# Performance work log

Hardware: AMD Instinct MI355X
Metric: run time of the kernel (lower is better)

The kernel has to match this reference:

```python
import jax, jax.numpy as jnp
import numpy as np

N_NODES = 100000
N_EDGES = 1600000
IN_CH = 16
HID = 128
N_LAYERS = 4
OUT_CH = 3


def setup_inputs() -> dict:
    key = jax.random.key(0)
    ks = jax.random.split(key, 8)
    x = jax.random.normal(ks[0], (N_NODES, IN_CH), dtype=jnp.float32)
    edge_index = jax.random.randint(ks[1], (2, N_EDGES), 0, N_NODES, dtype=jnp.int64)
    # glorot-ish scaled params
    enc_W = jax.random.normal(ks[2], (IN_CH, HID), dtype=jnp.float32) * (1.0 / np.sqrt(IN_CH))
    enc_b = jnp.zeros((HID,), dtype=jnp.float32)
    conv_W = jax.random.normal(ks[3], (N_LAYERS, HID, HID), dtype=jnp.float32) * (1.0 / np.sqrt(HID))
    conv_b = jnp.zeros((N_LAYERS, HID), dtype=jnp.float32)
    dec_W = jax.random.normal(ks[4], (HID, OUT_CH), dtype=jnp.float32) * (1.0 / np.sqrt(HID))
    dec_b = jnp.zeros((OUT_CH,), dtype=jnp.float32)
    return {"x": x, "edge_index": edge_index, "enc_W": enc_W, "enc_b": enc_b,
            "conv_W": conv_W, "conv_b": conv_b, "dec_W": dec_W, "dec_b": dec_b}


def _gcn_forward(x, edge_index, enc_W, enc_b, conv_W, conv_b, dec_W, dec_b):
    n = x.shape[0]
    # PyG GCNConv: add self-loops, symmetric deg^-1/2 normalization
    loops = jnp.arange(n, dtype=edge_index.dtype)
    src = jnp.concatenate([edge_index[0], loops])  # [E+N]
    dst = jnp.concatenate([edge_index[1], loops])  # [E+N]
    deg = jax.ops.segment_sum(jnp.ones_like(dst, dtype=x.dtype), dst, num_segments=n)
    dinv = jnp.where(deg > 0, jax.lax.rsqrt(deg), 0.0)
    norm = (dinv[src] * dinv[dst])[:, None]  # [E+N, 1]

    h = jax.nn.relu(x @ enc_W + enc_b)  # encoder + ReLU
    for l in range(conv_W.shape[0]):
        hw = h @ conv_W[l]                      # [N, H] transform
        msg = hw[src] * norm                    # gather + normalize
        h = jax.ops.segment_sum(msg, dst, num_segments=n) + conv_b[l]
        h = jax.nn.relu(h)
    return h @ dec_W + dec_b  # decoder [N, 3]


def reference(x, edge_index, enc_W, enc_b, conv_W, conv_b, dec_W, dec_b):
    return _gcn_forward(x, edge_index, enc_W, enc_b, conv_W, conv_b, dec_W, dec_b)
```

## Files before the change

kernel.cpp:

```cpp
#include <hip/hip_runtime.h>


typedef float f32x4 __attribute__((ext_vector_type(4)));
typedef _Float16 h8 __attribute__((ext_vector_type(8)));

#define BKT_CAP 6144


__global__ __launch_bounds__(256) void k_bin(const int* __restrict__ src, const int* __restrict__ dst,
                                             int* __restrict__ bcnt, unsigned* __restrict__ ebuf, int E, int NB) {
  __shared__ int hist[512];
  __shared__ int lofs[512];
  int tid = threadIdx.x;
  int base = blockIdx.x * 4096;
  for (int i = tid; i < NB; i += 256) hist[i] = 0;
  __syncthreads();
  unsigned rec[16];
  int bk[16];
#pragma unroll
  for (int j = 0; j < 16; j++) {
    int e = base + j * 256 + tid;
    bk[j] = -1;
    if (e < E) {
      int d = dst[e];
      rec[j] = ((unsigned)(d & 255) << 24) | (unsigned)src[e];
      bk[j] = d >> 8;
      atomicAdd(&hist[bk[j]], 1);
    }
  }
  __syncthreads();
  for (int i = tid; i < NB; i += 256) {
    int c = hist[i];
    lofs[i] = c ? atomicAdd(&bcnt[i], c) : 0;
    hist[i] = 0;
  }
  __syncthreads();
#pragma unroll
  for (int j = 0; j < 16; j++) {
    if (bk[j] >= 0) {
      int p = lofs[bk[j]] + atomicAdd(&hist[bk[j]], 1);
      if (p < BKT_CAP) ebuf[(size_t)bk[j] * BKT_CAP + p] = rec[j];
    }
  }
}

__global__ __launch_bounds__(512) void k_bscan(const int* __restrict__ bcnt, int* __restrict__ bbase,
                                               int* __restrict__ rp, int NB, int N, int E) {
  __shared__ int wsum[8];
  int tid = threadIdx.x;
  int v = (tid < NB) ? bcnt[tid] : 0;
  int l = tid & 63, w = tid >> 6;
  int s = v;
#pragma unroll
  for (int off = 1; off < 64; off <<= 1) { int t = __shfl_up(s, off); if (l >= off) s += t; }
  if (l == 63) wsum[w] = s;
  __syncthreads();
  int woff = 0;
  for (int i = 0; i < w; i++) woff += wsum[i];
  if (tid < NB) bbase[tid] = woff + s - v;
  if (tid == 0) rp[N] = E;
}

__global__ __launch_bounds__(256) void k_bfill(const unsigned* __restrict__ ebuf, const int* __restrict__ bcnt,
                                               const int* __restrict__ bbase, int* __restrict__ rp,
                                               float* __restrict__ dinv, int* __restrict__ col, int N) {
  __shared__ int h[256];
  __shared__ int wsum[4];
  int b = blockIdx.x, tid = threadIdx.x;
  h[tid] = 0;
  __syncthreads();
  int n = min(bcnt[b], BKT_CAP);
  int bb = bbase[b];
  const unsigned* eb = ebuf + (size_t)b * BKT_CAP;
  for (int i = tid; i < n; i += 256) atomicAdd(&h[eb[i] >> 24], 1);
  __syncthreads();
  int cntv = h[tid];
  int l = tid & 63, wv = tid >> 6;
  int s = cntv;
#pragma unroll
  for (int off = 1; off < 64; off <<= 1) { int t = __shfl_up(s, off); if (l >= off) s += t; }
  if (l == 63) wsum[wv] = s;
  __syncthreads();
  int woff = 0;
  for (int i = 0; i < wv; i++) woff += wsum[i];
  int lpre = woff + s - cntv;
  int d = (b << 8) + tid;
  if (d < N) {
    rp[d] = bb + lpre;
    dinv[d] = 1.0f / sqrtf((float)(cntv + 1));
  }
  __syncthreads();
  h[tid] = lpre;
  __syncthreads();
  for (int i = tid; i < n; i += 256) {
    unsigned r = eb[i];
    int dlow = r >> 24;
    int pos = bb + atomicAdd(&h[dlow], 1);
    col[pos] = (int)(r & 0xFFFFFFu);
  }
}

__global__ __launch_bounds__(128) void k_prep_w(const float* __restrict__ convW, _Float16* __restrict__ Whi,
                                                _Float16* __restrict__ Wlo) {
  int lk = blockIdx.x;
  int l = lk >> 7, k = lk & 127, c = threadIdx.x;
  float x = convW[((size_t)l * 128 + k) * 128 + c];
  _Float16 hi = (_Float16)x;
  _Float16 lo = (_Float16)((x - (float)hi) * 2048.0f);
  size_t o = ((size_t)l * 128 + c) * 128 + k;
  Whi[o] = hi;
  Wlo[o] = lo;
}


__global__ __launch_bounds__(256) void k_encoder(const float* __restrict__ x, const float* __restrict__ W,
                                                 const float* __restrict__ b, _Float16* __restrict__ H, int N) {
  int node = blockIdx.x * 2 + (threadIdx.x >> 7);
  int c = threadIdx.x & 127;
  if (node >= N) return;
  const float* xr = x + (size_t)node * 16;
  float acc = b[c];
#pragma unroll
  for (int k = 0; k < 16; k++) acc = fmaf(xr[k], W[k * 128 + c], acc);
  H[(size_t)node * 128 + c] = (_Float16)fmaxf(acc, 0.0f);
}

__global__ __launch_bounds__(512) void k_gemm_mfma(const _Float16* __restrict__ A, const _Float16* __restrict__ Whi,
                                                   const _Float16* __restrict__ Wlo, const float* __restrict__ dinv,
                                                   _Float16* __restrict__ B, int N) {
  __shared__ __align__(16) ushort lds[3 * 128 * 64];
  const int tid = threadIdx.x;
  const int row0 = blockIdx.x * 128;
  const int w = tid >> 6, l = tid & 63;
  const int wm = w >> 1, wn = w & 1;
  const int lr = l & 15, lg = l >> 4;

  f32x4 zero4 = {0.0f, 0.0f, 0.0f, 0.0f};
  f32x4 acc[2][4], acc2[2][4];
#pragma unroll
  for (int m = 0; m < 2; m++)
#pragma unroll
    for (int n = 0; n < 4; n++) { acc[m][n] = zero4; acc2[m][n] = zero4; }

  for (int half = 0; half < 2; half++) {
    uint4 v[6];
#pragma unroll
    for (int i = 0; i < 6; i++) {
      int g = tid + i * 512;
      int region = g >> 10;
      int idx = g & 1023;
      int row = idx >> 3;
      int c16 = idx & 7;
      const _Float16* srcb;
      int grow = row;
      bool valid = true;
      if (region == 0) { srcb = A; grow = row0 + row; valid = grow < N; }
      else if (region == 1) { srcb = Whi; }
      else { srcb = Wlo; }
      v[i] = valid ? *reinterpret_cast<const uint4*>(srcb + (size_t)grow * 128 + half * 64 + c16 * 8)
                   : uint4{0u, 0u, 0u, 0u};
    }
    if (half) __syncthreads();
#pragma unroll
    for (int i = 0; i < 6; i++) {
      int g = tid + i * 512;
      int region = g >> 10;
      int idx = g & 1023;
      int row = idx >> 3;
      int c16 = idx & 7;
      int byte_off = region * 16384 + ((row * 128 + c16 * 16) ^ ((row & 7) << 4));
      *reinterpret_cast<uint4*>(reinterpret_cast<char*>(lds) + byte_off) = v[i];
    }
    __syncthreads();

#pragma unroll
    for (int ksl = 0; ksl < 2; ksl++) {
      int kb = (ksl * 32 + lg * 8) * 2;
      h8 ah[2];
#pragma unroll
      for (int m = 0; m < 2; m++) {
        int row = wm * 32 + m * 16 + lr;
        int off = (row * 128 + kb) ^ ((row & 7) << 4);
        ah[m] = *reinterpret_cast<const h8*>(reinterpret_cast<char*>(lds) + off);
      }
      h8 wh[4], wl[4];
#pragma unroll
      for (int n = 0; n < 4; n++) {
        int colr = wn * 64 + n * 16 + lr;
        int off = (colr * 128 + kb) ^ ((colr & 7) << 4);
        wh[n] = *reinterpret_cast<const h8*>(reinterpret_cast<char*>(lds) + 16384 + off);
        wl[n] = *reinterpret_cast<const h8*>(reinterpret_cast<char*>(lds) + 32768 + off);
      }
#pragma unroll
      for (int m = 0; m < 2; m++)
#pragma unroll
        for (int n = 0; n < 4; n++) {
          acc2[m][n] = __builtin_amdgcn_mfma_f32_16x16x32_f16(ah[m], wl[n], acc2[m][n], 0, 0, 0);
          acc[m][n]  = __builtin_amdgcn_mfma_f32_16x16x32_f16(ah[m], wh[n], acc[m][n], 0, 0, 0);
        }
    }
  }

#pragma unroll
  for (int m = 0; m < 2; m++) {
    int rbase = row0 + wm * 32 + m * 16 + lg * 4;
#pragma unroll
    for (int r = 0; r < 4; r++) {
      int grow = rbase + r;
      if (grow < N) {
        float s = dinv[grow];
#pragma unroll
        for (int n = 0; n < 4; n++) {
          int colc = wn * 64 + n * 16 + lr;
          float val = acc[m][n][r] + 4.8828125e-4f * acc2[m][n][r];
          B[(size_t)grow * 128 + colc] = (_Float16)(val * s);
        }
      }
    }
  }
}

__global__ __launch_bounds__(256) void k_aggregate(const _Float16* __restrict__ B, const int* __restrict__ rp,
                                                   const int* __restrict__ col, const float* __restrict__ dinv,
                                                   const float* __restrict__ bias, _Float16* __restrict__ H,
                                                   const float* __restrict__ decW, const float* __restrict__ decb,
                                                   float* __restrict__ out, int last, int N) {
  int w = threadIdx.x >> 6, l = threadIdx.x & 63;
  int d = blockIdx.x * 4 + w;
  if (d >= N) return;
  int g = l >> 4, c16 = l & 15;
  int choff = c16 * 8;

  h8 z = {(_Float16)0, (_Float16)0, (_Float16)0, (_Float16)0,
          (_Float16)0, (_Float16)0, (_Float16)0, (_Float16)0};
  h8 a0 = z, a1 = z, a2 = z, a3 = z;

  if (g == 0)
    a1 += *reinterpret_cast<const h8*>(B + (size_t)d * 128 + choff);

  int e0 = rp[d], e1 = rp[d + 1];
  int len = e1 - e0;
  int q = (len + 3) >> 2;
  int a = e0 + g * q;
  int b = a + q; b = b < e1 ? b : e1;
  int i = a;
  for (; i + 3 < b; i += 4) {
    int s0 = col[i], s1 = col[i + 1], s2 = col[i + 2], s3 = col[i + 3];
    a0 += *reinterpret_cast<const h8*>(B + (size_t)s0 * 128 + choff);
    a1 += *reinterpret_cast<const h8*>(B + (size_t)s1 * 128 + choff);
    a2 += *reinterpret_cast<const h8*>(B + (size_t)s2 * 128 + choff);
    a3 += *reinterpret_cast<const h8*>(B + (size_t)s3 * 128 + choff);
  }
  if (i < b)     a0 += *reinterpret_cast<const h8*>(B + (size_t)col[i] * 128 + choff);
  if (i + 1 < b) a1 += *reinterpret_cast<const h8*>(B + (size_t)col[i + 1] * 128 + choff);
  if (i + 2 < b) a2 += *reinterpret_cast<const h8*>(B + (size_t)col[i + 2] * 128 + choff);

  h8 pacc = (a0 + a1) + (a2 + a3);

  float acc[8];
#pragma unroll
  for (int j = 0; j < 8; j++) acc[j] = (float)pacc[j];
#pragma unroll
  for (int j = 0; j < 8; j++) acc[j] += __shfl_xor(acc[j], 32);
#pragma unroll
  for (int j = 0; j < 8; j++) acc[j] += __shfl_xor(acc[j], 16);

  float dv = dinv[d];
  if (!last) {
    if (g == 0) {
      h8 ov;
#pragma unroll
      for (int j = 0; j < 8; j++)
        ov[j] = (_Float16)fmaxf(fmaf(dv, acc[j], bias[choff + j]), 0.0f);
      *reinterpret_cast<h8*>(&H[(size_t)d * 128 + choff]) = ov;
    }
  } else {
    float p0 = 0.f, p1 = 0.f, p2 = 0.f;
#pragma unroll
    for (int j = 0; j < 8; j++) {
      float o = fmaxf(fmaf(dv, acc[j], bias[choff + j]), 0.0f);
      int c = choff + j;
      p0 = fmaf(o, decW[c * 3 + 0], p0);
      p1 = fmaf(o, decW[c * 3 + 1], p1);
      p2 = fmaf(o, decW[c * 3 + 2], p2);
    }
#pragma unroll
    for (int off = 8; off > 0; off >>= 1) {
      p0 += __shfl_down(p0, off);
      p1 += __shfl_down(p1, off);
      p2 += __shfl_down(p2, off);
    }
    if (l == 0) {
      out[(size_t)d * 3 + 0] = p0 + decb[0];
      out[(size_t)d * 3 + 1] = p1 + decb[1];
      out[(size_t)d * 3 + 2] = p2 + decb[2];
    }
  }
}

extern "C" void kernel_launch(void* const* d_in, const int* in_sizes, int n_in,
                              void* d_out, int out_size, void* d_ws, size_t ws_size,
                              hipStream_t stream) {
  const float* x     = (const float*)d_in[0];
  const int*   ei    = (const int*)d_in[1];
  const float* encW  = (const float*)d_in[2];
  const float* encb  = (const float*)d_in[3];
  const float* convW = (const float*)d_in[4];
  const float* convb = (const float*)d_in[5];
  const float* decW  = (const float*)d_in[6];
  const float* decb  = (const float*)d_in[7];
  const int N = in_sizes[0] / 16;
  const int E = in_sizes[1] / 2;
  const int L = in_sizes[4] / (128 * 128);
  const int* src = ei;
  const int* dst = ei + E;
  const int NB = (N + 255) >> 8;

  char* p = (char*)d_ws;
  auto alloc = [&](size_t bytes) -> void* {
    void* q = (void*)p;
    p += (bytes + 255) & ~(size_t)255;
    return q;
  };
  int*       rp     = (int*)alloc((size_t)(N + 1) * 4);
  int*       bcnt   = (int*)alloc((size_t)NB * 4);
  int*       bbase  = (int*)alloc((size_t)NB * 4);
  float*     dinv   = (float*)alloc((size_t)N * 4);
  int*       colA   = (int*)alloc((size_t)E * 4);
  _Float16*  Hh     = (_Float16*)alloc((size_t)N * 128 * 2);
  size_t bh_bytes   = (size_t)N * 128 * 2;
  size_t ebuf_bytes = (size_t)NB * BKT_CAP * 4;
  void*  bh_union   = alloc(bh_bytes > ebuf_bytes ? bh_bytes : ebuf_bytes);
  _Float16* Bh      = (_Float16*)bh_union;
  unsigned* ebuf    = (unsigned*)bh_union;
  _Float16*  Whi    = (_Float16*)alloc((size_t)L * 128 * 128 * 2);
  _Float16*  Wlo    = (_Float16*)alloc((size_t)L * 128 * 128 * 2);

  hipMemsetAsync(bcnt, 0, (size_t)NB * 4, stream);
  k_bin<<<(E + 4095) / 4096, 256, 0, stream>>>(src, dst, bcnt, ebuf, E, NB);
  k_bscan<<<1, 512, 0, stream>>>(bcnt, bbase, rp, NB, N, E);
  k_bfill<<<NB, 256, 0, stream>>>(ebuf, bcnt, bbase, rp, dinv, colA, N);
  k_prep_w<<<L * 128, 128, 0, stream>>>(convW, Whi, Wlo);
  k_encoder<<<(N + 1) / 2, 256, 0, stream>>>(x, encW, encb, Hh, N);
  int gblocks = (N + 127) / 128;
  for (int l = 0; l < L; l++) {
    k_gemm_mfma<<<gblocks, 512, 0, stream>>>(Hh, Whi + (size_t)l * 128 * 128,
                                             Wlo + (size_t)l * 128 * 128, dinv, Bh, N);
    k_aggregate<<<(N + 3) / 4, 256, 0, stream>>>(Bh, rp, colA, dinv, convb + l * 128, Hh,
                                                 decW, decb, (float*)d_out, (l == L - 1) ? 1 : 0, N);
  }
}
```

Before: 531.7 us.

## Fuse aggregation and GEMM per layer using aggregate-then-transform order

Reorders each GCN layer to aggregate the pre-scaled features first (A·H) and then multiply by W, which the linearity of the layer allows. Gather and GEMM are fused into one kernel, with the aggregated rows kept in LDS. This removes the intermediate B buffer round trip through global memory and one launch per layer. The encoder and layer epilogue now store dinv-prescaled features, and the decoder reads from LDS. In exchange, each 512-thread block gathers 128 rows serially with 16 lanes per row. It also uses 48KB of LDS, which may lower occupancy and latency hiding for the irregular gather, and fp16 accumulation order changes.

New measurement: 531.1 us. Within noise of the previous version (-0.1%).

```diff
diff --git a/kernel.cpp b/kernel.cpp
--- a/kernel.cpp
+++ b/kernel.cpp
@@ -112,9 +112,9 @@
   Wlo[o] = lo;
 }
 
-
 __global__ __launch_bounds__(256) void k_encoder(const float* __restrict__ x, const float* __restrict__ W,
-                                                 const float* __restrict__ b, _Float16* __restrict__ H, int N) {
+                                                 const float* __restrict__ b, const float* __restrict__ dinv,
+                                                 _Float16* __restrict__ Hp, int N) {
   int node = blockIdx.x * 2 + (threadIdx.x >> 7);
   int c = threadIdx.x & 127;
   if (node >= N) return;
@@ -122,19 +122,63 @@
   float acc = b[c];
 #pragma unroll
   for (int k = 0; k < 16; k++) acc = fmaf(xr[k], W[k * 128 + c], acc);
-  H[(size_t)node * 128 + c] = (_Float16)fmaxf(acc, 0.0f);
-}
-
-__global__ __launch_bounds__(512) void k_gemm_mfma(const _Float16* __restrict__ A, const _Float16* __restrict__ Whi,
-                                                   const _Float16* __restrict__ Wlo, const float* __restrict__ dinv,
-                                                   _Float16* __restrict__ B, int N) {
-  __shared__ __align__(16) ushort lds[3 * 128 * 64];
+  Hp[(size_t)node * 128 + c] = (_Float16)(dinv[node] * fmaxf(acc, 0.0f));
+}
+
+__global__ __launch_bounds__(512, 4) void k_layer(const _Float16* __restrict__ Hp, const int* __restrict__ rp,
+                                                  const int* __restrict__ col, const float* __restrict__ dinv,
+                                                  const _Float16* __restrict__ Whi, const _Float16* __restrict__ Wlo,
+                                                  const float* __restrict__ bias, _Float16* __restrict__ Hn,
+                                                  const float* __restrict__ decW, const float* __restrict__ decb,
+                                                  float* __restrict__ out, int last, int N) {
+  __shared__ __align__(16) ushort ldsM[128 * 128];
+  __shared__ __align__(16) ushort ldsW[128 * 64];
+  char* mB = reinterpret_cast<char*>(ldsM);
+  char* wB = reinterpret_cast<char*>(ldsW);
   const int tid = threadIdx.x;
   const int row0 = blockIdx.x * 128;
+
+  {
+    int grp = tid >> 4, ln = tid & 15;
+#pragma unroll
+    for (int t = 0; t < 4; t++) {
+      int lrow = grp * 4 + t;
+      int d = row0 + lrow;
+      int moff = (lrow * 256 + ln * 16) ^ ((lrow & 7) << 4);
+      h8 z = {(_Float16)0, (_Float16)0, (_Float16)0, (_Float16)0,
+              (_Float16)0, (_Float16)0, (_Float16)0, (_Float16)0};
+      if (d < N) {
+        h8 a0 = z, a1 = z, a2 = z, a3 = z;
+        a0 += *reinterpret_cast<const h8*>(Hp + (size_t)d * 128 + ln * 8);
+        int e0 = rp[d], e1 = rp[d + 1];
+        int i = e0;
+        for (; i + 3 < e1; i += 4) {
+          int s0 = col[i], s1 = col[i + 1], s2 = col[i + 2], s3 = col[i + 3];
+          a0 += *reinterpret_cast<const h8*>(Hp + (size_t)s0 * 128 + ln * 8);
+          a1 += *reinterpret_cast<const h8*>(Hp + (size_t)s1 * 128 + ln * 8);
+          a2 += *reinterpret_cast<const h8*>(Hp + (size_t)s2 * 128 + ln * 8);
+          a3 += *reinterpret_cast<const h8*>(Hp + (size_t)s3 * 128 + ln * 8);
+        }
+        if (i < e1)     a1 += *reinterpret_cast<const h8*>(Hp + (size_t)col[i] * 128 + ln * 8);
+        if (i + 1 < e1) a2 += *reinterpret_cast<const h8*>(Hp + (size_t)col[i + 1] * 128 + ln * 8);
+        if (i + 2 < e1) a3 += *reinterpret_cast<const h8*>(Hp + (size_t)col[i + 2] * 128 + ln * 8);
+        h8 m;
+#pragma unroll
+        for (int j = 0; j < 8; j++) {
+          float f = ((float)a0[j] + (float)a1[j]) + ((float)a2[j] + (float)a3[j]);
+          m[j] = (_Float16)f;
+        }
+        *reinterpret_cast<h8*>(mB + moff) = m;
+      } else {
+        *reinterpret_cast<h8*>(mB + moff) = z;
+      }
+    }
+  }
+  __syncthreads();
+
   const int w = tid >> 6, l = tid & 63;
   const int wm = w >> 1, wn = w & 1;
   const int lr = l & 15, lg = l >> 4;
-
   f32x4 zero4 = {0.0f, 0.0f, 0.0f, 0.0f};
   f32x4 acc[2][4], acc2[2][4];
 #pragma unroll
@@ -143,157 +187,107 @@
     for (int n = 0; n < 4; n++) { acc[m][n] = zero4; acc2[m][n] = zero4; }
 
   for (int half = 0; half < 2; half++) {
-    uint4 v[6];
-#pragma unroll
-    for (int i = 0; i < 6; i++) {
-      int g = tid + i * 512;
-      int region = g >> 10;
-      int idx = g & 1023;
-      int row = idx >> 3;
-      int c16 = idx & 7;
-      const _Float16* srcb;
-      int grow = row;
-      bool valid = true;
-      if (region == 0) { srcb = A; grow = row0 + row; valid = grow < N; }
-      else if (region == 1) { srcb = Whi; }
-      else { srcb = Wlo; }
-      v[i] = valid ? *reinterpret_cast<const uint4*>(srcb + (size_t)grow * 128 + half * 64 + c16 * 8)
-                   : uint4{0u, 0u, 0u, 0u};
-    }
-    if (half) __syncthreads();
-#pragma unroll
-    for (int i = 0; i < 6; i++) {
-      int g = tid + i * 512;
-      int region = g >> 10;
-      int idx = g & 1023;
-      int row = idx >> 3;
-      int c16 = idx & 7;
-      int byte_off = region * 16384 + ((row * 128 + c16 * 16) ^ ((row & 7) << 4));
-      *reinterpret_cast<uint4*>(reinterpret_cast<char*>(lds) + byte_off) = v[i];
-    }
-    __syncthreads();
-
-#pragma unroll
-    for (int ksl = 0; ksl < 2; ksl++) {
-      int kb = (ksl * 32 + lg * 8) * 2;
-      h8 ah[2];
-#pragma unroll
-      for (int m = 0; m < 2; m++) {
-        int row = wm * 32 + m * 16 + lr;
-        int off = (row * 128 + kb) ^ ((row & 7) << 4);
-        ah[m] = *reinterpret_cast<const h8*>(reinterpret_cast<char*>(lds) + off);
-      }
-      h8 wh[4], wl[4];
-#pragma unroll
-      for (int n = 0; n < 4; n++) {
-        int colr = wn * 64 + n * 16 + lr;
-        int off = (colr * 128 + kb) ^ ((colr & 7) << 4);
-        wh[n] = *reinterpret_cast<const h8*>(reinterpret_cast<char*>(lds) + 16384 + off);
-        wl[n] = *reinterpret_cast<const h8*>(reinterpret_cast<char*>(lds) + 32768 + off);
-      }
-#pragma unroll
-      for (int m = 0; m < 2; m++)
+#pragma unroll
+    for (int plane = 0; plane < 2; plane++) {
+      if (half | plane) __syncthreads();
+      const _Float16* Wp = plane ? Wlo : Whi;
+#pragma unroll
+      for (int i = 0; i < 2; i++) {
+        int g = tid + i * 512;
+        int c = g >> 3, c16 = g & 7;
+        uint4 v = *reinterpret_cast<const uint4*>(Wp + (size_t)c * 128 + half * 64 + c16 * 8);
+        *reinterpret_cast<uint4*>(wB + ((c * 128 + c16 * 16) ^ ((c & 7) << 4))) = v;
+      }
+      __syncthreads();
+#pragma unroll
+      for (int ksl = 0; ksl < 2; ksl++) {
+        int kb = (ksl * 32 + lg * 8) * 2;
+        h8 ah[2];
+#pragma unroll
+        for (int m = 0; m < 2; m++) {
+          int row = wm * 32 + m * 16 + lr;
+          ah[m] = *reinterpret_cast<const h8*>(mB + ((row * 256 + half * 128 + kb) ^ ((row & 7) << 4)));
+        }
+        h8 wf[4];
 #pragma unroll
         for (int n = 0; n < 4; n++) {
-          acc2[m][n] = __builtin_amdgcn_mfma_f32_16x16x32_f16(ah[m], wl[n], acc2[m][n], 0, 0, 0);
-          acc[m][n]  = __builtin_amdgcn_mfma_f32_16x16x32_f16(ah[m], wh[n], acc[m][n], 0, 0, 0);
-        }
-    }
-  }
-
+          int colr = wn * 64 + n * 16 + lr;
+          wf[n] = *reinterpret_cast<const h8*>(wB + ((colr * 128 + kb) ^ ((colr & 7) << 4)));
+        }
+        if (plane == 0) {
+#pragma unroll
+          for (int m = 0; m < 2; m++)
+#pragma unroll
+            for (int n = 0; n < 4; n++)
+              acc[m][n] = __builtin_amdgcn_mfma_f32_16x16x32_f16(ah[m], wf[n], acc[m][n], 0, 0, 0);
+        } else {
+#pragma unroll
+          for (int m = 0; m < 2; m++)
+#pragma unroll
+            for (int n = 0; n < 4; n++)
+              acc2[m][n] = __builtin_amdgcn_mfma_f32_16x16x32_f16(ah[m], wf[n], acc2[m][n], 0, 0, 0);
+        }
+      }
+    }
+  }
+
+  if (last) __syncthreads();
 #pragma unroll
   for (int m = 0; m < 2; m++) {
-    int rbase = row0 + wm * 32 + m * 16 + lg * 4;
+    int lbase = wm * 32 + m * 16 + lg * 4;
 #pragma unroll
     for (int r = 0; r < 4; r++) {
-      int grow = rbase + r;
+      int lrow = lbase + r;
+      int grow = row0 + lrow;
       if (grow < N) {
-        float s = dinv[grow];
+        float dv = dinv[grow];
 #pragma unroll
         for (int n = 0; n < 4; n++) {
           int colc = wn * 64 + n * 16 + lr;
           float val = acc[m][n][r] + 4.8828125e-4f * acc2[m][n][r];
-          B[(size_t)grow * 128 + colc] = (_Float16)(val * s);
-        }
-      }
-    }
-  }
-}
-
-__global__ __launch_bounds__(256) void k_aggregate(const _Float16* __restrict__ B, const int* __restrict__ rp,
-                                                   const int* __restrict__ col, const float* __restrict__ dinv,
-                                                   const float* __restrict__ bias, _Float16* __restrict__ H,
-                                                   const float* __restrict__ decW, const float* __restrict__ decb,
-                                                   float* __restrict__ out, int last, int N) {
-  int w = threadIdx.x >> 6, l = threadIdx.x & 63;
-  int d = blockIdx.x * 4 + w;
-  if (d >= N) return;
-  int g = l >> 4, c16 = l & 15;
-  int choff = c16 * 8;
-
-  h8 z = {(_Float16)0, (_Float16)0, (_Float16)0, (_Float16)0,
-          (_Float16)0, (_Float16)0, (_Float16)0, (_Float16)0};
-  h8 a0 = z, a1 = z, a2 = z, a3 = z;
-
-  if (g == 0)
-    a1 += *reinterpret_cast<const h8*>(B + (size_t)d * 128 + choff);
-
-  int e0 = rp[d], e1 = rp[d + 1];
-  int len = e1 - e0;
-  int q = (len + 3) >> 2;
-  int a = e0 + g * q;
-  int b = a + q; b = b < e1 ? b : e1;
-  int i = a;
-  for (; i + 3 < b; i += 4) {
-    int s0 = col[i], s1 = col[i + 1], s2 = col[i + 2], s3 = col[i + 3];
-    a0 += *reinterpret_cast<const h8*>(B + (size_t)s0 * 128 + choff);
-    a1 += *reinterpret_cast<const h8*>(B + (size_t)s1 * 128 + choff);
-    a2 += *reinterpret_cast<const h8*>(B + (size_t)s2 * 128 + choff);
-    a3 += *reinterpret_cast<const h8*>(B + (size_t)s3 * 128 + choff);
-  }
-  if (i < b)     a0 += *reinterpret_cast<const h8*>(B + (size_t)col[i] * 128 + choff);
-  if (i + 1 < b) a1 += *reinterpret_cast<const h8*>(B + (size_t)col[i + 1] * 128 + choff);
-  if (i + 2 < b) a2 += *reinterpret_cast<const h8*>(B + (size_t)col[i + 2] * 128 + choff);
-
-  h8 pacc = (a0 + a1) + (a2 + a3);
-
-  float acc[8];
-#pragma unroll
-  for (int j = 0; j < 8; j++) acc[j] = (float)pacc[j];
-#pragma unroll
-  for (int j = 0; j < 8; j++) acc[j] += __shfl_xor(acc[j], 32);
-#pragma unroll
-  for (int j = 0; j < 8; j++) acc[j] += __shfl_xor(acc[j], 16);
-
-  float dv = dinv[d];
-  if (!last) {
-    if (g == 0) {
-      h8 ov;
-#pragma unroll
-      for (int j = 0; j < 8; j++)
-        ov[j] = (_Float16)fmaxf(fmaf(dv, acc[j], bias[choff + j]), 0.0f);
-      *reinterpret_cast<h8*>(&H[(size_t)d * 128 + choff]) = ov;
-    }
-  } else {
-    float p0 = 0.f, p1 = 0.f, p2 = 0.f;
-#pragma unroll
-    for (int j = 0; j < 8; j++) {
-      float o = fmaxf(fmaf(dv, acc[j], bias[choff + j]), 0.0f);
-      int c = choff + j;
-      p0 = fmaf(o, decW[c * 3 + 0], p0);
-      p1 = fmaf(o, decW[c * 3 + 1], p1);
-      p2 = fmaf(o, decW[c * 3 + 2], p2);
-    }
-#pragma unroll
-    for (int off = 8; off > 0; off >>= 1) {
-      p0 += __shfl_down(p0, off);
-      p1 += __shfl_down(p1, off);
-      p2 += __shfl_down(p2, off);
-    }
-    if (l == 0) {
-      out[(size_t)d * 3 + 0] = p0 + decb[0];
-      out[(size_t)d * 3 + 1] = p1 + decb[1];
-      out[(size_t)d * 3 + 2] = p2 + decb[2];
+          float h = fmaxf(fmaf(dv, val, bias[colc]), 0.0f);
+          if (!last) {
+            Hn[(size_t)grow * 128 + colc] = (_Float16)(dv * h);
+          } else {
+            _Float16 hf = (_Float16)h;
+            *reinterpret_cast<ushort*>(mB + ((lrow * 256 + colc * 2) ^ ((lrow & 7) << 4))) =
+                *reinterpret_cast<ushort*>(&hf);
+          }
+        }
+      }
+    }
+  }
+
+  if (last) {
+    __syncthreads();
+    int grp = tid >> 4, ln = tid & 15;
+#pragma unroll
+    for (int t = 0; t < 4; t++) {
+      int lrow = grp * 4 + t;
+      int d = row0 + lrow;
+      if (d < N) {
+        h8 hv = *reinterpret_cast<const h8*>(mB + ((lrow * 256 + ln * 16) ^ ((lrow & 7) << 4)));
+        float p0 = 0.f, p1 = 0.f, p2 = 0.f;
+#pragma unroll
+        for (int j = 0; j < 8; j++) {
+          int c = ln * 8 + j;
+          float o = (float)hv[j];
+          p0 = fmaf(o, decW[c * 3 + 0], p0);
+          p1 = fmaf(o, decW[c * 3 + 1], p1);
+          p2 = fmaf(o, decW[c * 3 + 2], p2);
+        }
+#pragma unroll
+        for (int off = 8; off > 0; off >>= 1) {
+          p0 += __shfl_xor(p0, off);
+          p1 += __shfl_xor(p1, off);
+          p2 += __shfl_xor(p2, off);
+        }
+        if (ln == 0) {
+          out[(size_t)d * 3 + 0] = p0 + decb[0];
+          out[(size_t)d * 3 + 1] = p1 + decb[1];
+          out[(size_t)d * 3 + 2] = p2 + decb[2];
+        }
+      }
     }
   }
 }
@@ -327,12 +321,12 @@
   int*       bbase  = (int*)alloc((size_t)NB * 4);
   float*     dinv   = (float*)alloc((size_t)N * 4);
   int*       colA   = (int*)alloc((size_t)E * 4);
-  _Float16*  Hh     = (_Float16*)alloc((size_t)N * 128 * 2);
-  size_t bh_bytes   = (size_t)N * 128 * 2;
+  _Float16*  HA     = (_Float16*)alloc((size_t)N * 128 * 2);
+  size_t hb_bytes   = (size_t)N * 128 * 2;
   size_t ebuf_bytes = (size_t)NB * BKT_CAP * 4;
-  void*  bh_union   = alloc(bh_bytes > ebuf_bytes ? bh_bytes : ebuf_bytes);
-  _Float16* Bh      = (_Float16*)bh_union;
-  unsigned* ebuf    = (unsigned*)bh_union;
+  void*  hb_union   = alloc(hb_bytes > ebuf_bytes ? hb_bytes : ebuf_bytes);
+  _Float16* HB      = (_Float16*)hb_union;
+  unsigned* ebuf    = (unsigned*)hb_union;
   _Float16*  Whi    = (_Float16*)alloc((size_t)L * 128 * 128 * 2);
   _Float16*  Wlo    = (_Float16*)alloc((size_t)L * 128 * 128 * 2);
 
@@ -341,12 +335,15 @@
   k_bscan<<<1, 512, 0, stream>>>(bcnt, bbase, rp, NB, N, E);
   k_bfill<<<NB, 256, 0, stream>>>(ebuf, bcnt, bbase, rp, dinv, colA, N);
   k_prep_w<<<L * 128, 128, 0, stream>>>(convW, Whi, Wlo);
-  k_encoder<<<(N + 1) / 2, 256, 0, stream>>>(x, encW, encb, Hh, N);
+  k_encoder<<<(N + 1) / 2, 256, 0, stream>>>(x, encW, encb, dinv, HA, N);
   int gblocks = (N + 127) / 128;
+  _Float16* Hp = HA;
+  _Float16* Hn = HB;
   for (int l = 0; l < L; l++) {
-    k_gemm_mfma<<<gblocks, 512, 0, stream>>>(Hh, Whi + (size_t)l * 128 * 128,
-                                             Wlo + (size_t)l * 128 * 128, dinv, Bh, N);
-    k_aggregate<<<(N + 3) / 4, 256, 0, stream>>>(Bh, rp, colA, dinv, convb + l * 128, Hh,
-                                                 decW, decb, (float*)d_out, (l == L - 1) ? 1 : 0, N);
-  }
-}
+    int last = (l == L - 1) ? 1 : 0;
+    k_layer<<<gblocks, 512, 0, stream>>>(Hp, rp, colA, dinv, Whi + (size_t)l * 128 * 128,
+                                         Wlo + (size_t)l * 128 * 128, convb + l * 128, Hn,
+                                         decW, decb, (float*)d_out, last, N);
+    _Float16* t = Hp; Hp = Hn; Hn = t;
+  }
+}
```
